# Kernel tuning notes

Hardware: AMD Instinct MI355X
Metric: run time of the kernel (lower is better)

## Reference

```python
import jax, jax.numpy as jnp
import numpy as np

N = 100000
IN_DIM = 256
HID = 128
E = 1600000


def _gcn_conv(x, W, b, src, dst, n_nodes):
    """PyG GCNConv: add self-loops, symmetric normalization, linear transform."""
    xw = x @ W  # [N, H]
    loop = jnp.arange(n_nodes, dtype=src.dtype)
    s = jnp.concatenate([src, loop])  # sources (j)
    d = jnp.concatenate([dst, loop])  # targets (i)
    ones = jnp.ones(s.shape[0], dtype=x.dtype)
    deg = jax.ops.segment_sum(ones, d, num_segments=n_nodes)  # in-degree incl. self-loop
    dinv = jnp.where(deg > 0, jax.lax.rsqrt(deg), 0.0)
    norm = dinv[s] * dinv[d]  # [E+N]
    msgs = xw[s] * norm[:, None]  # gather + scale
    out = jax.ops.segment_sum(msgs, d, num_segments=n_nodes)  # scatter-add at targets
    return out + b


def setup_inputs() -> dict:
    key = jax.random.key(0)
    ks = jax.random.split(key, 12)
    x = jax.random.normal(ks[0], (N, IN_DIM), dtype=jnp.float32)
    edge_index = jax.random.randint(ks[1], (2, E), 0, N, dtype=jnp.int64)
    h_node = jax.random.uniform(ks[2], (N,), dtype=jnp.float32)
    # learned params (glorot-ish scale)
    W1 = jax.random.normal(ks[3], (IN_DIM, HID), dtype=jnp.float32) / np.sqrt(IN_DIM)
    b1 = jnp.zeros((HID,), dtype=jnp.float32)
    W2 = jax.random.normal(ks[4], (HID, HID), dtype=jnp.float32) / np.sqrt(HID)
    b2 = jnp.zeros((HID,), dtype=jnp.float32)
    Wc = jax.random.normal(ks[5], (HID, 2), dtype=jnp.float32) / np.sqrt(HID)
    bc = jnp.zeros((2,), dtype=jnp.float32)
    Wf = jax.random.normal(ks[6], (HID, 2), dtype=jnp.float32) / np.sqrt(HID)
    bf = jnp.zeros((2,), dtype=jnp.float32)
    return {"x": x, "edge_index": edge_index, "h_node": h_node,
            "W1": W1, "b1": b1, "W2": W2, "b2": b2,
            "Wc": Wc, "bc": bc, "Wf": Wf, "bf": bf}


def reference(x, edge_index, h_node, W1, b1, W2, b2, Wc, bc, Wf, bf):
    src, dst = edge_index[0], edge_index[1]
    h1 = jax.nn.relu(_gcn_conv(x, W1, b1, src, dst, x.shape[0]))      # [N, HID]
    logits_coarse = h1 @ Wc + bc                                      # [N, 2]
    alpha = h_node[:, None]                                           # [N, 1]
    h2 = jax.nn.relu(_gcn_conv(h1, W2, b2, src, dst, x.shape[0]))     # [N, HID]
    h2_adaptive = alpha * h2 + (1.0 - alpha) * h1
    logits_fine = h2_adaptive @ Wf + bf                               # [N, 2]
    return 0.5 * logits_coarse + 0.5 * logits_fine
```

## Files before the change

### kernel.cpp

```cpp
#include <hip/hip_runtime.h>


#define HID 128
#define SHIFT 9
#define RANGE 512
#define MAXB 256
#define TILE 4096

typedef __bf16 bf16x8 __attribute__((ext_vector_type(8)));
typedef float  f32x4  __attribute__((ext_vector_type(4)));
typedef float  f32x2  __attribute__((ext_vector_type(2)));

__device__ __forceinline__ unsigned short f2bf(float x) {
    unsigned int b = __float_as_uint(x);
    b += 0x7fffu + ((b >> 16) & 1u);
    return (unsigned short)(b >> 16);
}
__device__ __forceinline__ float bflo(unsigned int u) { return __uint_as_float(u << 16); }
__device__ __forceinline__ float bfhi(unsigned int u) { return __uint_as_float(u & 0xffff0000u); }
__device__ __forceinline__ unsigned packbf(float a, float b) {
    return (unsigned)f2bf(a) | ((unsigned)f2bf(b) << 16);
}


__global__ __launch_bounds__(256)
void bincount_kernel(const int* __restrict__ dst, int* __restrict__ bin_counts,
                     int E, int NB) {
    __shared__ int h[MAXB];
    for (int i = threadIdx.x; i < NB; i += 256) h[i] = 0;
    __syncthreads();
    const int base = blockIdx.x * TILE;
#pragma unroll
    for (int j = 0; j < TILE; j += 256) {
        int e = base + j + threadIdx.x;
        if (e < E) atomicAdd(&h[((unsigned)dst[e]) >> SHIFT], 1);
    }
    __syncthreads();
    for (int i = threadIdx.x; i < NB; i += 256) {
        int v = h[i];
        if (v) atomicAdd(&bin_counts[i], v);
    }
}

__global__ void binscan_kernel(const int* __restrict__ bin_counts,
                               int* __restrict__ bin_off, int* __restrict__ bin_cur, int NB) {
    __shared__ int sh[MAXB];
    const int t = threadIdx.x;
    int v = (t < NB) ? bin_counts[t] : 0;
    sh[t] = v;
    __syncthreads();
    for (int s = 1; s < 256; s <<= 1) {
        int x = (t >= s) ? sh[t - s] : 0;
        __syncthreads();
        sh[t] += x;
        __syncthreads();
    }
    if (t < NB) {
        int ex = sh[t] - v;
        bin_off[t] = ex;
        bin_cur[t] = ex;
    }
}

__global__ __launch_bounds__(256)
void stage_kernel(const int* __restrict__ src, const int* __restrict__ dst,
                  int* __restrict__ bin_cur, unsigned* __restrict__ pairs, int E) {
    __shared__ int sh_hist[MAXB];
    __shared__ int sh_off[MAXB];
    __shared__ int sh_ex[MAXB];
    __shared__ int sh_gbase[MAXB];
    __shared__ uint2 stg[TILE];
    const int t = threadIdx.x;
    const int base = blockIdx.x * TILE;
    const int cnt = min(TILE, E - base);

    for (int i = t; i < MAXB; i += 256) sh_hist[i] = 0;
    __syncthreads();

    int s[16], d[16], r[16];
#pragma unroll
    for (int j = 0; j < 16; ++j) {
        const int k = j * 256 + t;
        if (k < cnt) {
            s[j] = src[base + k];
            d[j] = dst[base + k];
            r[j] = atomicAdd(&sh_hist[((unsigned)d[j]) >> SHIFT], 1);
        }
    }
    __syncthreads();

    const int hv = sh_hist[t];
    sh_off[t] = hv;
    __syncthreads();
    for (int st = 1; st < 256; st <<= 1) {
        int x = (t >= st) ? sh_off[t - st] : 0;
        __syncthreads();
        sh_off[t] += x;
        __syncthreads();
    }
    sh_ex[t] = sh_off[t] - hv;
    if (hv > 0) sh_gbase[t] = atomicAdd(&bin_cur[t], hv);
    __syncthreads();

#pragma unroll
    for (int j = 0; j < 16; ++j) {
        const int k = j * 256 + t;
        if (k < cnt) {
            int b = ((unsigned)d[j]) >> SHIFT;
            stg[sh_ex[b] + r[j]] = make_uint2((unsigned)s[j], (unsigned)d[j]);
        }
    }
    __syncthreads();

    for (int i = t; i < cnt; i += 256) {
        uint2 p = stg[i];
        int b = (int)(p.y >> SHIFT);
        unsigned w = ((p.y & (RANGE - 1)) << 23) | p.x;
        pairs[sh_gbase[b] + (i - sh_ex[b])] = w;
    }
}

__global__ __launch_bounds__(256)
void binrowp_kernel(const unsigned* __restrict__ pairs, const int* __restrict__ bin_off,
                    float* __restrict__ dinv, int* __restrict__ rowp,
                    int N, int NB, int E) {
    __shared__ int c[RANGE];
    __shared__ int sh[256];
    const int b = blockIdx.x;
    const int t = threadIdx.x;
    const int nb = b << SHIFT;
    const int nr = min(RANGE, N - nb);
    for (int i = t; i < RANGE; i += 256) c[i] = 0;
    __syncthreads();
    const int lo = bin_off[b];
    const int hi = (b + 1 < NB) ? bin_off[b + 1] : E;
    for (int i = lo + t; i < hi; i += 256)
        atomicAdd(&c[pairs[i] >> 23], 1);
    __syncthreads();
    const int v0 = c[2 * t], v1 = c[2 * t + 1];
    const int pr = v0 + v1;
    sh[t] = pr;
    __syncthreads();
    for (int s = 1; s < 256; s <<= 1) {
        int x = (t >= s) ? sh[t - s] : 0;
        __syncthreads();
        sh[t] += x;
        __syncthreads();
    }
    const int ex = sh[t] - pr + lo;
    if (2 * t < nr) {
        rowp[nb + 2 * t] = ex;
        dinv[nb + 2 * t] = rsqrtf((float)(v0 + 1));
    }
    if (2 * t + 1 < nr) {
        rowp[nb + 2 * t + 1] = ex + v0;
        dinv[nb + 2 * t + 1] = rsqrtf((float)(v1 + 1));
    }
    if (b == 0 && t == 0) rowp[N] = E;
}

__global__ __launch_bounds__(256)
void fine_kernel(const unsigned* __restrict__ pairs, const int* __restrict__ bin_off,
                 const int* __restrict__ rowp, const float* __restrict__ dinv,
                 unsigned* __restrict__ colv1, int N, int NB, int E) {
    __shared__ int cur[RANGE];
    const int b = blockIdx.x;
    const int nb = b << SHIFT;
    const int nr = min(RANGE, N - nb);
    for (int i = threadIdx.x; i < nr; i += 256) cur[i] = rowp[nb + i];
    __syncthreads();
    const int lo = bin_off[b];
    const int hi = (b + 1 < NB) ? bin_off[b + 1] : E;
    for (int i = lo + threadIdx.x; i < hi; i += 256) {
        unsigned w = pairs[i];
        unsigned s = w & 0x7fffffu;
        int pos = atomicAdd(&cur[w >> 23], 1);
        unsigned w15 = __float2uint_rn(dinv[s] * 32767.0f);
        colv1[pos] = (s << 15) | w15;
    }
}

__global__ void prep_kernel(const float* __restrict__ W1, const float* __restrict__ W2,
                            unsigned short* __restrict__ wt1, unsigned short* __restrict__ wt2,
                            int K1, int* __restrict__ bin_counts) {
    int idx = blockIdx.x * 256 + threadIdx.x;
    if (idx < MAXB) bin_counts[idx] = 0;
    if (idx < 128 * K1) {
        int nn = idx / K1, k = idx - nn * K1;
        wt1[(size_t)nn * K1 + k] = f2bf(W1[(size_t)k * 128 + nn]);
    }
    if (idx < 128 * 128) {
        int nn = idx >> 7, k = idx & 127;
        wt2[(size_t)nn * 128 + k] = f2bf(W2[(size_t)k * 128 + nn]);
    }
}

template <bool A_BF16, int K>
__global__ __launch_bounds__(256)
void gemm_kernel(const void* __restrict__ Aptr, const unsigned short* __restrict__ Wt,
                 unsigned short* __restrict__ Out, int nrows) {
    constexpr int NIT  = K / 32;
    constexpr int DEPTH = (NIT < 4) ? NIT : 4;
    constexpr int HK   = (K > 128) ? (K / 2) : K;
    constexpr int CHH  = HK / 8;
    constexpr int PH   = K / HK;
    constexpr int NITP = HK / 32;
    __shared__ uint4 sB[128 * CHH];

    const int tid  = threadIdx.x;
    const int wave = tid >> 6;
    const int lane = tid & 63;
    const int q = lane >> 4;
    const int r = lane & 15;

    const int wrow = blockIdx.x * 64 + wave * 16;
    const size_t row0 = (size_t)min(wrow + r, nrows - 1);

    const unsigned short* A16 = (const unsigned short*)Aptr;
    const float*          A32 = (const float*)Aptr;

    f32x4 acc[8];
#pragma unroll
    for (int c = 0; c < 8; ++c) acc[c] = (f32x4){0.f, 0.f, 0.f, 0.f};

    bf16x8 preb[DEPTH];
    float4 pref[DEPTH][2];

#pragma unroll
    for (int i = 0; i < DEPTH; ++i) {
        const int kk = i * 32 + q * 8;
        if (A_BF16) {
            preb[i] = *reinterpret_cast<const bf16x8*>(A16 + row0 * K + kk);
        } else {
            pref[i][0] = *reinterpret_cast<const float4*>(A32 + row0 * K + kk);
            pref[i][1] = *reinterpret_cast<const float4*>(A32 + row0 * K + kk + 4);
        }
    }

#pragma unroll
    for (int ph = 0; ph < PH; ++ph) {
        if (ph) __syncthreads();
        for (int idx = tid; idx < 128 * CHH; idx += 256) {
            const int col = idx / CHH;
            const int kc  = idx & (CHH - 1);
            const uint4 v = *reinterpret_cast<const uint4*>(
                Wt + (size_t)col * K + ph * HK + kc * 8);
            sB[col * CHH + (kc ^ (col & (CHH - 1)))] = v;
        }
        __syncthreads();

#pragma unroll
        for (int itp = 0; itp < NITP; ++itp) {
            const int git  = ph * NITP + itp;
            const int slot = git % DEPTH;

            bf16x8 bcur[8];
#pragma unroll
            for (int c = 0; c < 8; ++c) {
                const int col = c * 16 + r;
                const int chunk = (itp * 4 + q) ^ (col & (CHH - 1));
                bcur[c] = *reinterpret_cast<const bf16x8*>(&sB[col * CHH + chunk]);
            }

            bf16x8 afrag;
            if (A_BF16) {
                afrag = preb[slot];
            } else {
                const float4 x0 = pref[slot][0];
                const float4 x1 = pref[slot][1];
                bf16x8 a;
                a[0] = (__bf16)x0.x; a[1] = (__bf16)x0.y; a[2] = (__bf16)x0.z; a[3] = (__bf16)x0.w;
                a[4] = (__bf16)x1.x; a[5] = (__bf16)x1.y; a[6] = (__bf16)x1.z; a[7] = (__bf16)x1.w;
                afrag = a;
            }

            if (git + DEPTH < NIT) {
                const int kk2 = (git + DEPTH) * 32 + q * 8;
                if (A_BF16) {
                    preb[slot] = *reinterpret_cast<const bf16x8*>(A16 + row0 * K + kk2);
                } else {
                    pref[slot][0] = *reinterpret_cast<const float4*>(A32 + row0 * K + kk2);
                    pref[slot][1] = *reinterpret_cast<const float4*>(A32 + row0 * K + kk2 + 4);
                }
            }

#pragma unroll
            for (int c = 0; c < 8; ++c)
                acc[c] = __builtin_amdgcn_mfma_f32_16x16x32_bf16(afrag, bcur[c], acc[c], 0, 0, 0);
        }
    }

#pragma unroll
    for (int v = 0; v < 4; ++v) {
        const int row = wrow + q * 4 + v;
        if (row < nrows) {
#pragma unroll
            for (int c = 0; c < 8; ++c)
                Out[(size_t)row * 128 + c * 16 + r] = f2bf(acc[c][v]);
        }
    }
}


#define AGG_ISSUE(g, TBL)                                                     \
    if ((g) * 4 < cnt) {                                                      \
        _Pragma("unroll")                                                     \
        for (int j = 0; j < 4; ++j) {                                         \
            const int sl = (g) * 4 + j;                                       \
            const unsigned cg = (unsigned)__shfl((int)cw, qb + sl);           \
            wt[sl] = (float)(cg & 0x7fffu) * (1.0f / 32767.0f);               \
            pf[sl] = *reinterpret_cast<const uint4*>(                         \
                (const char*)(TBL) + (((cg >> 15) << 8) + coff));             \
        }                                                                     \
    }

#define AGG_CONS(g)                                                          \
    if ((g) * 4 < cnt) {                                                     \
        _Pragma("unroll")                                                    \
        for (int j = 0; j < 4; ++j) {                                        \
            const int sl = (g) * 4 + j;                                      \
            const float w = wt[sl];                                          \
            const uint4 uu = pf[sl];                                         \
            A0 += (f32x2){bflo(uu.x), bfhi(uu.x)} * w;                       \
            A1 += (f32x2){bflo(uu.y), bfhi(uu.y)} * w;                       \
            A2 += (f32x2){bflo(uu.z), bfhi(uu.z)} * w;                       \
            A3 += (f32x2){bflo(uu.w), bfhi(uu.w)} * w;                       \
        }                                                                    \
    }

#define AGG_EDGE_LOOP(TBL)                                                   \
    unsigned cw = (beg + c < end) ? colv1[beg + c] : 0u;                     \
    for (int base = beg; base < end; base += 16) {                           \
        const int cnt = end - base;                                          \
        AGG_ISSUE(0, TBL) AGG_ISSUE(1, TBL) AGG_ISSUE(2, TBL) AGG_ISSUE(3, TBL) \
        unsigned cw_next = 0u;                                               \
        if (base + 16 + c < end) cw_next = colv1[base + 16 + c];             \
        AGG_CONS(0) AGG_CONS(1) AGG_CONS(2) AGG_CONS(3)                      \
        cw = cw_next;                                                        \
    }

__device__ __forceinline__ f32x2 __shfl_xor(f32x2 v, int m) {
    return (f32x2){__shfl_xor(v[0], m), __shfl_xor(v[1], m)};
}

__global__ __launch_bounds__(256)
void agg1_kernel(const unsigned short* __restrict__ xw, const unsigned* __restrict__ colv1,
                 const int* __restrict__ rowp, const float* __restrict__ dinv,
                 const float* __restrict__ b1, const float* __restrict__ Wc,
                 const float* __restrict__ bc, uint4* __restrict__ h1,
                 float* __restrict__ outp, int n) {
    const int node = blockIdx.x * 16 + (threadIdx.x >> 4);
    if (node >= n) return;
    const int lane = threadIdx.x & 63;
    const int c    = lane & 15;
    const int qb   = lane & 48;
    const unsigned coff = (unsigned)c << 4;
    const float di = dinv[node];
    const int beg = rowp[node], end = rowp[node + 1];

    const uint4 su = *reinterpret_cast<const uint4*>(
        (const char*)xw + (((unsigned)node << 8) + coff));

    f32x2 A0 = {0.f,0.f}, A1 = {0.f,0.f}, A2 = {0.f,0.f}, A3 = {0.f,0.f};
    uint4 pf[16];
    float wt[16];

    AGG_EDGE_LOOP(xw)

    A0 += (f32x2){bflo(su.x), bfhi(su.x)} * di;
    A1 += (f32x2){bflo(su.y), bfhi(su.y)} * di;
    A2 += (f32x2){bflo(su.z), bfhi(su.z)} * di;
    A3 += (f32x2){bflo(su.w), bfhi(su.w)} * di;

    const float4 bb0 = reinterpret_cast<const float4*>(b1)[2*c];
    const float4 bb1 = reinterpret_cast<const float4*>(b1)[2*c + 1];
    float a0 = fmaxf(A0[0]*di + bb0.x, 0.f), a1 = fmaxf(A0[1]*di + bb0.y, 0.f);
    float a2 = fmaxf(A1[0]*di + bb0.z, 0.f), a3 = fmaxf(A1[1]*di + bb0.w, 0.f);
    float a4 = fmaxf(A2[0]*di + bb1.x, 0.f), a5 = fmaxf(A2[1]*di + bb1.y, 0.f);
    float a6 = fmaxf(A3[0]*di + bb1.z, 0.f), a7 = fmaxf(A3[1]*di + bb1.w, 0.f);

    h1[((unsigned)node << 4) + c] =
        make_uint4(packbf(a0,a1), packbf(a2,a3), packbf(a4,a5), packbf(a6,a7));

    const float4 w0 = reinterpret_cast<const float4*>(Wc)[4*c];
    const float4 w1 = reinterpret_cast<const float4*>(Wc)[4*c + 1];
    const float4 w2 = reinterpret_cast<const float4*>(Wc)[4*c + 2];
    const float4 w3 = reinterpret_cast<const float4*>(Wc)[4*c + 3];
    float c0 = a0*w0.x + a1*w0.z + a2*w1.x + a3*w1.z
             + a4*w2.x + a5*w2.z + a6*w3.x + a7*w3.z;
    float c1 = a0*w0.y + a1*w0.w + a2*w1.y + a3*w1.w
             + a4*w2.y + a5*w2.w + a6*w3.y + a7*w3.w;
#pragma unroll
    for (int off = 1; off < 16; off <<= 1) {
        c0 += __shfl_xor(c0, off);
        c1 += __shfl_xor(c1, off);
    }
    if (c == 0) {
        outp[2 * (size_t)node]     = 0.5f * (c0 + bc[0]);
        outp[2 * (size_t)node + 1] = 0.5f * (c1 + bc[1]);
    }
}

__global__ __launch_bounds__(256)
void agg2_kernel(const unsigned short* __restrict__ xw2, const uint4* __restrict__ h1,
                 const unsigned* __restrict__ colv1, const int* __restrict__ rowp,
                 const float* __restrict__ dinv, const float* __restrict__ b2,
                 const float* __restrict__ Wf, const float* __restrict__ bfv,
                 const float* __restrict__ hnode, float* __restrict__ outp, int n) {
    const int node = blockIdx.x * 16 + (threadIdx.x >> 4);
    if (node >= n) return;
    const int lane = threadIdx.x & 63;
    const int c    = lane & 15;
    const int qb   = lane & 48;
    const unsigned coff = (unsigned)c << 4;
    const float di = dinv[node];
    const int beg = rowp[node], end = rowp[node + 1];

    const uint4 su = *reinterpret_cast<const uint4*>(
        (const char*)xw2 + (((unsigned)node << 8) + coff));

    f32x2 A0 = {0.f,0.f}, A1 = {0.f,0.f}, A2 = {0.f,0.f}, A3 = {0.f,0.f};
    uint4 pf[16];
    float wt[16];

    AGG_EDGE_LOOP(xw2)

    A0 += (f32x2){bflo(su.x), bfhi(su.x)} * di;
    A1 += (f32x2){bflo(su.y), bfhi(su.y)} * di;
    A2 += (f32x2){bflo(su.z), bfhi(su.z)} * di;
    A3 += (f32x2){bflo(su.w), bfhi(su.w)} * di;

    const float4 bb0 = reinterpret_cast<const float4*>(b2)[2*c];
    const float4 bb1 = reinterpret_cast<const float4*>(b2)[2*c + 1];
    float h20 = fmaxf(A0[0]*di + bb0.x, 0.f), h21 = fmaxf(A0[1]*di + bb0.y, 0.f);
    float h22 = fmaxf(A1[0]*di + bb0.z, 0.f), h23 = fmaxf(A1[1]*di + bb0.w, 0.f);
    float h24 = fmaxf(A2[0]*di + bb1.x, 0.f), h25 = fmaxf(A2[1]*di + bb1.y, 0.f);
    float h26 = fmaxf(A3[0]*di + bb1.z, 0.f), h27 = fmaxf(A3[1]*di + bb1.w, 0.f);

    const float alpha = hnode[node];
    const float beta  = 1.f - alpha;
    const uint4 hh = h1[((unsigned)node << 4) + c];
    const float ha0 = alpha*h20 + beta*bflo(hh.x);
    const float ha1 = alpha*h21 + beta*bfhi(hh.x);
    const float ha2 = alpha*h22 + beta*bflo(hh.y);
    const float ha3 = alpha*h23 + beta*bfhi(hh.y);
    const float ha4 = alpha*h24 + beta*bflo(hh.z);
    const float ha5 = alpha*h25 + beta*bfhi(hh.z);
    const float ha6 = alpha*h26 + beta*bflo(hh.w);
    const float ha7 = alpha*h27 + beta*bfhi(hh.w);

    const float4 w0 = reinterpret_cast<const float4*>(Wf)[4*c];
    const float4 w1 = reinterpret_cast<const float4*>(Wf)[4*c + 1];
    const float4 w2 = reinterpret_cast<const float4*>(Wf)[4*c + 2];
    const float4 w3 = reinterpret_cast<const float4*>(Wf)[4*c + 3];
    float f0 = ha0*w0.x + ha1*w0.z + ha2*w1.x + ha3*w1.z
             + ha4*w2.x + ha5*w2.z + ha6*w3.x + ha7*w3.z;
    float f1 = ha0*w0.y + ha1*w0.w + ha2*w1.y + ha3*w1.w
             + ha4*w2.y + ha5*w2.w + ha6*w3.y + ha7*w3.w;
#pragma unroll
    for (int off = 1; off < 16; off <<= 1) {
        f0 += __shfl_xor(f0, off);
        f1 += __shfl_xor(f1, off);
    }
    if (c == 0) {
        outp[2 * (size_t)node]     += 0.5f * (f0 + bfv[0]);
        outp[2 * (size_t)node + 1] += 0.5f * (f1 + bfv[1]);
    }
}


extern "C" void kernel_launch(void* const* d_in, const int* in_sizes, int n_in,
                              void* d_out, int out_size, void* d_ws, size_t ws_size,
                              hipStream_t stream) {
    const float* x     = (const float*)d_in[0];
    const int*   ei    = (const int*)d_in[1];
    const float* hnode = (const float*)d_in[2];
    const float* W1    = (const float*)d_in[3];
    const float* b1    = (const float*)d_in[4];
    const float* W2    = (const float*)d_in[5];
    const float* b2    = (const float*)d_in[6];
    const float* Wc    = (const float*)d_in[7];
    const float* bc    = (const float*)d_in[8];
    const float* Wf    = (const float*)d_in[9];
    const float* bfv   = (const float*)d_in[10];

    const int N  = in_sizes[2];
    const int E  = in_sizes[1] / 2;
    const int K1 = in_sizes[3] / HID;
    const int NB = (N + RANGE - 1) >> SHIFT;
    const int* srcv = ei;
    const int* dstv = ei + E;
    float* outp = (float*)d_out;

    char* ws = (char*)d_ws;
    size_t off = 0;
    auto alloc = [&](size_t bytes) -> char* {
        char* p = ws + off;
        off += (bytes + 255) & ~(size_t)255;
        return p;
    };
    unsigned short* xw       = (unsigned short*)alloc((size_t)N * HID * 2);
    unsigned short* h1       = (unsigned short*)alloc((size_t)N * HID * 2);
    float*          dinv     = (float*)alloc((size_t)N * 4);
    int*            rowp     = (int*)alloc((size_t)(N + 1) * 4);
    unsigned*       colv1    = (unsigned*)alloc((size_t)E * 4);
    unsigned*       pairs    = (unsigned*)alloc((size_t)E * 4);
    int*            bin_counts = (int*)alloc(MAXB * 4);
    int*            bin_off    = (int*)alloc(MAXB * 4);
    int*            bin_cur    = (int*)alloc(MAXB * 4);
    unsigned short* wt1      = (unsigned short*)alloc((size_t)HID * K1 * 2);
    unsigned short* wt2      = (unsigned short*)alloc((size_t)HID * HID * 2);

    prep_kernel<<<(HID * K1 + 255) / 256, 256, 0, stream>>>(W1, W2, wt1, wt2, K1, bin_counts);

    const int ntiles = (E + TILE - 1) / TILE;
    bincount_kernel<<<ntiles, 256, 0, stream>>>(dstv, bin_counts, E, NB);
    binscan_kernel<<<1, 256, 0, stream>>>(bin_counts, bin_off, bin_cur, NB);
    stage_kernel<<<ntiles, 256, 0, stream>>>(srcv, dstv, bin_cur, pairs, E);
    binrowp_kernel<<<NB, 256, 0, stream>>>(pairs, bin_off, dinv, rowp, N, NB, E);
    fine_kernel<<<NB, 256, 0, stream>>>(pairs, bin_off, rowp, dinv, colv1, N, NB, E);

    gemm_kernel<false, 256><<<(N + 63) / 64, 256, 0, stream>>>((const void*)x, wt1, xw, N);
    agg1_kernel<<<(N + 15) / 16, 256, 0, stream>>>(xw, colv1, rowp, dinv,
                                                   b1, Wc, bc, (uint4*)h1, outp, N);
    gemm_kernel<true, 128><<<(N + 63) / 64, 256, 0, stream>>>((const void*)h1, wt2, xw, N);
    agg2_kernel<<<(N + 15) / 16, 256, 0, stream>>>(xw, (const uint4*)h1, colv1,
                                                   rowp, dinv, b2, Wf, bfv, hnode, outp, N);
}
```

Before: 375.8 us.

## Use 8 lanes per node with double-buffered edge gathers in aggregation

Both aggregation kernels now map each node to 8 lanes instead of 16, so each lane gathers 32 bytes (two uint4) per neighbor row and 32 nodes fit in a block. The edge loop becomes a two-stage software pipeline with ping-pong prefetch buffers and sched_barriers, and it recomputes weights from the shuffled column word instead of storing them. The aim is to halve the lanes per node, which doubles node-level parallelism per wave, and to overlap gather latency with accumulation. The trade-off is higher register pressure from 16 prefetched uint4 plus 16 accumulators, which may reduce occupancy.

Result: slower. 393.1 us (+4.6%).

```diff
diff --git a/kernel.cpp b/kernel.cpp
--- a/kernel.cpp
+++ b/kernel.cpp
@@ -302,41 +302,61 @@
 }
 
 
-#define AGG_ISSUE(g, TBL)                                                     \
-    if ((g) * 4 < cnt) {                                                      \
+#define AGG_ISS(PF, CW, t)                                                    \
+    if (((t) << 2) < me) {                                                    \
         _Pragma("unroll")                                                     \
         for (int j = 0; j < 4; ++j) {                                         \
-            const int sl = (g) * 4 + j;                                       \
-            const unsigned cg = (unsigned)__shfl((int)cw, qb + sl);           \
-            wt[sl] = (float)(cg & 0x7fffu) * (1.0f / 32767.0f);               \
-            pf[sl] = *reinterpret_cast<const uint4*>(                         \
-                (const char*)(TBL) + (((cg >> 15) << 8) + coff));             \
+            const unsigned cg = (unsigned)__shfl((int)(CW), gb + j);          \
+            const char* p = (const char*)tbl + (((cg >> 15) << 8) + coff);    \
+            PF[2 * j]     = *reinterpret_cast<const uint4*>(p);               \
+            PF[2 * j + 1] = *reinterpret_cast<const uint4*>(p + 16);          \
         }                                                                     \
     }
 
-#define AGG_CONS(g)                                                          \
-    if ((g) * 4 < cnt) {                                                     \
-        _Pragma("unroll")                                                    \
-        for (int j = 0; j < 4; ++j) {                                        \
-            const int sl = (g) * 4 + j;                                      \
-            const float w = wt[sl];                                          \
-            const uint4 uu = pf[sl];                                         \
-            A0 += (f32x2){bflo(uu.x), bfhi(uu.x)} * w;                       \
-            A1 += (f32x2){bflo(uu.y), bfhi(uu.y)} * w;                       \
-            A2 += (f32x2){bflo(uu.z), bfhi(uu.z)} * w;                       \
-            A3 += (f32x2){bflo(uu.w), bfhi(uu.w)} * w;                       \
-        }                                                                    \
-    }
-
-#define AGG_EDGE_LOOP(TBL)                                                   \
-    unsigned cw = (beg + c < end) ? colv1[beg + c] : 0u;                     \
-    for (int base = beg; base < end; base += 16) {                           \
-        const int cnt = end - base;                                          \
-        AGG_ISSUE(0, TBL) AGG_ISSUE(1, TBL) AGG_ISSUE(2, TBL) AGG_ISSUE(3, TBL) \
-        unsigned cw_next = 0u;                                               \
-        if (base + 16 + c < end) cw_next = colv1[base + 16 + c];             \
-        AGG_CONS(0) AGG_CONS(1) AGG_CONS(2) AGG_CONS(3)                      \
-        cw = cw_next;                                                        \
+#define AGG_CNS(PF, CW, t)                                                    \
+    if (((t) << 2) < me) {                                                    \
+        _Pragma("unroll")                                                     \
+        for (int j = 0; j < 4; ++j) {                                         \
+            const unsigned cg = (unsigned)__shfl((int)(CW), gb + j);          \
+            const float w = (float)(cg & 0x7fffu) * (1.0f / 32767.0f);        \
+            const uint4 u0 = PF[2 * j];                                       \
+            const uint4 u1 = PF[2 * j + 1];                                   \
+            A0 += (f32x2){bflo(u0.x), bfhi(u0.x)} * w;                        \
+            A1 += (f32x2){bflo(u0.y), bfhi(u0.y)} * w;                        \
+            A2 += (f32x2){bflo(u0.z), bfhi(u0.z)} * w;                        \
+            A3 += (f32x2){bflo(u0.w), bfhi(u0.w)} * w;                        \
+            A4 += (f32x2){bflo(u1.x), bfhi(u1.x)} * w;                        \
+            A5 += (f32x2){bflo(u1.y), bfhi(u1.y)} * w;                        \
+            A6 += (f32x2){bflo(u1.z), bfhi(u1.z)} * w;                        \
+            A7 += (f32x2){bflo(u1.w), bfhi(u1.w)} * w;                        \
+        }                                                                     \
+    }
+
+#define AGG_EDGE_LOOP(TBL)                                                    \
+    const unsigned short* tbl = (TBL);                                        \
+    const int me = end - beg;                                                 \
+    auto ldcv = [&](int t) -> unsigned {                                      \
+        const int idx = beg + (t << 2) + (c8 & 3);                            \
+        return (idx < end) ? colv1[idx] : 0u;                                 \
+    };                                                                        \
+    uint4 pfA[8], pfB[8];                                                     \
+    unsigned cw0 = ldcv(0);                                                   \
+    unsigned cw1 = ldcv(1);                                                   \
+    AGG_ISS(pfA, cw0, 0)                                                      \
+    const int mych = (me + 3) >> 2;                                           \
+    for (int t = 0; t < mych; t += 2) {                                       \
+        const unsigned cw2 = ldcv(t + 2);                                     \
+        __builtin_amdgcn_sched_barrier(0);                                    \
+        AGG_ISS(pfB, cw1, t + 1)                                              \
+        __builtin_amdgcn_sched_barrier(0);                                    \
+        AGG_CNS(pfA, cw0, t)                                                  \
+        const unsigned cw3 = ldcv(t + 3);                                     \
+        __builtin_amdgcn_sched_barrier(0);                                    \
+        AGG_ISS(pfA, cw2, t + 2)                                              \
+        __builtin_amdgcn_sched_barrier(0);                                    \
+        AGG_CNS(pfB, cw1, t + 1)                                              \
+        __builtin_amdgcn_sched_barrier(0);                                    \
+        cw0 = cw2; cw1 = cw3;                                                 \
     }
 
 __device__ __forceinline__ f32x2 __shfl_xor(f32x2 v, int m) {
@@ -349,53 +369,66 @@
                  const float* __restrict__ b1, const float* __restrict__ Wc,
                  const float* __restrict__ bc, uint4* __restrict__ h1,
                  float* __restrict__ outp, int n) {
-    const int node = blockIdx.x * 16 + (threadIdx.x >> 4);
+    const int node = blockIdx.x * 32 + (threadIdx.x >> 3);
     if (node >= n) return;
     const int lane = threadIdx.x & 63;
-    const int c    = lane & 15;
-    const int qb   = lane & 48;
-    const unsigned coff = (unsigned)c << 4;
+    const int c8   = lane & 7;
+    const int gb   = lane & 56;
+    const unsigned coff = (unsigned)c8 << 5;
     const float di = dinv[node];
     const int beg = rowp[node], end = rowp[node + 1];
 
-    const uint4 su = *reinterpret_cast<const uint4*>(
-        (const char*)xw + (((unsigned)node << 8) + coff));
+    const char* sp = (const char*)xw + (((unsigned)node << 8) + coff);
+    const uint4 su0 = *reinterpret_cast<const uint4*>(sp);
+    const uint4 su1 = *reinterpret_cast<const uint4*>(sp + 16);
 
     f32x2 A0 = {0.f,0.f}, A1 = {0.f,0.f}, A2 = {0.f,0.f}, A3 = {0.f,0.f};
-    uint4 pf[16];
-    float wt[16];
+    f32x2 A4 = {0.f,0.f}, A5 = {0.f,0.f}, A6 = {0.f,0.f}, A7 = {0.f,0.f};
 
     AGG_EDGE_LOOP(xw)
 
-    A0 += (f32x2){bflo(su.x), bfhi(su.x)} * di;
-    A1 += (f32x2){bflo(su.y), bfhi(su.y)} * di;
-    A2 += (f32x2){bflo(su.z), bfhi(su.z)} * di;
-    A3 += (f32x2){bflo(su.w), bfhi(su.w)} * di;
-
-    const float4 bb0 = reinterpret_cast<const float4*>(b1)[2*c];
-    const float4 bb1 = reinterpret_cast<const float4*>(b1)[2*c + 1];
-    float a0 = fmaxf(A0[0]*di + bb0.x, 0.f), a1 = fmaxf(A0[1]*di + bb0.y, 0.f);
-    float a2 = fmaxf(A1[0]*di + bb0.z, 0.f), a3 = fmaxf(A1[1]*di + bb0.w, 0.f);
-    float a4 = fmaxf(A2[0]*di + bb1.x, 0.f), a5 = fmaxf(A2[1]*di + bb1.y, 0.f);
-    float a6 = fmaxf(A3[0]*di + bb1.z, 0.f), a7 = fmaxf(A3[1]*di + bb1.w, 0.f);
-
-    h1[((unsigned)node << 4) + c] =
+    A0 += (f32x2){bflo(su0.x), bfhi(su0.x)} * di;
+    A1 += (f32x2){bflo(su0.y), bfhi(su0.y)} * di;
+    A2 += (f32x2){bflo(su0.z), bfhi(su0.z)} * di;
+    A3 += (f32x2){bflo(su0.w), bfhi(su0.w)} * di;
+    A4 += (f32x2){bflo(su1.x), bfhi(su1.x)} * di;
+    A5 += (f32x2){bflo(su1.y), bfhi(su1.y)} * di;
+    A6 += (f32x2){bflo(su1.z), bfhi(su1.z)} * di;
+    A7 += (f32x2){bflo(su1.w), bfhi(su1.w)} * di;
+
+    const float4* b4 = reinterpret_cast<const float4*>(b1);
+    const float4 bb0 = b4[4*c8], bb1 = b4[4*c8+1], bb2 = b4[4*c8+2], bb3 = b4[4*c8+3];
+    float a0  = fmaxf(A0[0]*di + bb0.x, 0.f), a1  = fmaxf(A0[1]*di + bb0.y, 0.f);
+    float a2  = fmaxf(A1[0]*di + bb0.z, 0.f), a3  = fmaxf(A1[1]*di + bb0.w, 0.f);
+    float a4  = fmaxf(A2[0]*di + bb1.x, 0.f), a5  = fmaxf(A2[1]*di + bb1.y, 0.f);
+    float a6  = fmaxf(A3[0]*di + bb1.z, 0.f), a7  = fmaxf(A3[1]*di + bb1.w, 0.f);
+    float a8  = fmaxf(A4[0]*di + bb2.x, 0.f), a9  = fmaxf(A4[1]*di + bb2.y, 0.f);
+    float a10 = fmaxf(A5[0]*di + bb2.z, 0.f), a11 = fmaxf(A5[1]*di + bb2.w, 0.f);
+    float a12 = fmaxf(A6[0]*di + bb3.x, 0.f), a13 = fmaxf(A6[1]*di + bb3.y, 0.f);
+    float a14 = fmaxf(A7[0]*di + bb3.z, 0.f), a15 = fmaxf(A7[1]*di + bb3.w, 0.f);
+
+    h1[((unsigned)node << 4) + 2*c8] =
         make_uint4(packbf(a0,a1), packbf(a2,a3), packbf(a4,a5), packbf(a6,a7));
-
-    const float4 w0 = reinterpret_cast<const float4*>(Wc)[4*c];
-    const float4 w1 = reinterpret_cast<const float4*>(Wc)[4*c + 1];
-    const float4 w2 = reinterpret_cast<const float4*>(Wc)[4*c + 2];
-    const float4 w3 = reinterpret_cast<const float4*>(Wc)[4*c + 3];
-    float c0 = a0*w0.x + a1*w0.z + a2*w1.x + a3*w1.z
-             + a4*w2.x + a5*w2.z + a6*w3.x + a7*w3.z;
-    float c1 = a0*w0.y + a1*w0.w + a2*w1.y + a3*w1.w
-             + a4*w2.y + a5*w2.w + a6*w3.y + a7*w3.w;
-#pragma unroll
-    for (int off = 1; off < 16; off <<= 1) {
+    h1[((unsigned)node << 4) + 2*c8 + 1] =
+        make_uint4(packbf(a8,a9), packbf(a10,a11), packbf(a12,a13), packbf(a14,a15));
+
+    const float4* w4 = reinterpret_cast<const float4*>(Wc);
+    float c0 = 0.f, c1 = 0.f;
+    {
+        const float av[16] = {a0,a1,a2,a3,a4,a5,a6,a7,a8,a9,a10,a11,a12,a13,a14,a15};
+#pragma unroll
+        for (int j = 0; j < 8; ++j) {
+            const float4 w = w4[8*c8 + j];
+            c0 += av[2*j]*w.x + av[2*j+1]*w.z;
+            c1 += av[2*j]*w.y + av[2*j+1]*w.w;
+        }
+    }
+#pragma unroll
+    for (int off = 1; off < 8; off <<= 1) {
         c0 += __shfl_xor(c0, off);
         c1 += __shfl_xor(c1, off);
     }
-    if (c == 0) {
+    if (c8 == 0) {
         outp[2 * (size_t)node]     = 0.5f * (c0 + bc[0]);
         outp[2 * (size_t)node + 1] = 0.5f * (c1 + bc[1]);
     }
@@ -407,62 +440,73 @@
                  const float* __restrict__ dinv, const float* __restrict__ b2,
                  const float* __restrict__ Wf, const float* __restrict__ bfv,
                  const float* __restrict__ hnode, float* __restrict__ outp, int n) {
-    const int node = blockIdx.x * 16 + (threadIdx.x >> 4);
+    const int node = blockIdx.x * 32 + (threadIdx.x >> 3);
     if (node >= n) return;
     const int lane = threadIdx.x & 63;
-    const int c    = lane & 15;
-    const int qb   = lane & 48;
-    const unsigned coff = (unsigned)c << 4;
+    const int c8   = lane & 7;
+    const int gb   = lane & 56;
+    const unsigned coff = (unsigned)c8 << 5;
     const float di = dinv[node];
     const int beg = rowp[node], end = rowp[node + 1];
 
-    const uint4 su = *reinterpret_cast<const uint4*>(
-        (const char*)xw2 + (((unsigned)node << 8) + coff));
+    const char* sp = (const char*)xw2 + (((unsigned)node << 8) + coff);
+    const uint4 su0 = *reinterpret_cast<const uint4*>(sp);
+    const uint4 su1 = *reinterpret_cast<const uint4*>(sp + 16);
 
     f32x2 A0 = {0.f,0.f}, A1 = {0.f,0.f}, A2 = {0.f,0.f}, A3 = {0.f,0.f};
-    uint4 pf[16];
-    float wt[16];
+    f32x2 A4 = {0.f,0.f}, A5 = {0.f,0.f}, A6 = {0.f,0.f}, A7 = {0.f,0.f};
 
     AGG_EDGE_LOOP(xw2)
 
-    A0 += (f32x2){bflo(su.x), bfhi(su.x)} * di;
-    A1 += (f32x2){bflo(su.y), bfhi(su.y)} * di;
-    A2 += (f32x2){bflo(su.z), bfhi(su.z)} * di;
-    A3 += (f32x2){bflo(su.w), bfhi(su.w)} * di;
-
-    const float4 bb0 = reinterpret_cast<const float4*>(b2)[2*c];
-    const float4 bb1 = reinterpret_cast<const float4*>(b2)[2*c + 1];
-    float h20 = fmaxf(A0[0]*di + bb0.x, 0.f), h21 = fmaxf(A0[1]*di + bb0.y, 0.f);
-    float h22 = fmaxf(A1[0]*di + bb0.z, 0.f), h23 = fmaxf(A1[1]*di + bb0.w, 0.f);
-    float h24 = fmaxf(A2[0]*di + bb1.x, 0.f), h25 = fmaxf(A2[1]*di + bb1.y, 0.f);
-    float h26 = fmaxf(A3[0]*di + bb1.z, 0.f), h27 = fmaxf(A3[1]*di + bb1.w, 0.f);
+    A0 += (f32x2){bflo(su0.x), bfhi(su0.x)} * di;
+    A1 += (f32x2){bflo(su0.y), bfhi(su0.y)} * di;
+    A2 += (f32x2){bflo(su0.z), bfhi(su0.z)} * di;
+    A3 += (f32x2){bflo(su0.w), bfhi(su0.w)} * di;
+    A4 += (f32x2){bflo(su1.x), bfhi(su1.x)} * di;
+    A5 += (f32x2){bflo(su1.y), bfhi(su1.y)} * di;
+    A6 += (f32x2){bflo(su1.z), bfhi(su1.z)} * di;
+    A7 += (f32x2){bflo(su1.w), bfhi(su1.w)} * di;
+
+    const float4* b4 = reinterpret_cast<const float4*>(b2);
+    const float4 bb0 = b4[4*c8], bb1 = b4[4*c8+1], bb2 = b4[4*c8+2], bb3 = b4[4*c8+3];
+    float h2v[16];
+    h2v[0]  = fmaxf(A0[0]*di + bb0.x, 0.f); h2v[1]  = fmaxf(A0[1]*di + bb0.y, 0.f);
+    h2v[2]  = fmaxf(A1[0]*di + bb0.z, 0.f); h2v[3]  = fmaxf(A1[1]*di + bb0.w, 0.f);
+    h2v[4]  = fmaxf(A2[0]*di + bb1.x, 0.f); h2v[5]  = fmaxf(A2[1]*di + bb1.y, 0.f);
+    h2v[6]  = fmaxf(A3[0]*di + bb1.z, 0.f); h2v[7]  = fmaxf(A3[1]*di + bb1.w, 0.f);
+    h2v[8]  = fmaxf(A4[0]*di + bb2.x, 0.f); h2v[9]  = fmaxf(A4[1]*di + bb2.y, 0.f);
+    h2v[10] = fmaxf(A5[0]*di + bb2.z, 0.f); h2v[11] = fmaxf(A5[1]*di + bb2.w, 0.f);
+    h2v[12] = fmaxf(A6[0]*di + bb3.x, 0.f); h2v[13] = fmaxf(A6[1]*di + bb3.y, 0.f);
+    h2v[14] = fmaxf(A7[0]*di + bb3.z, 0.f); h2v[15] = fmaxf(A7[1]*di + bb3.w, 0.f);
 
     const float alpha = hnode[node];
     const float beta  = 1.f - alpha;
-    const uint4 hh = h1[((unsigned)node << 4) + c];
-    const float ha0 = alpha*h20 + beta*bflo(hh.x);
-    const float ha1 = alpha*h21 + beta*bfhi(hh.x);
-    const float ha2 = alpha*h22 + beta*bflo(hh.y);
-    const float ha3 = alpha*h23 + beta*bfhi(hh.y);
-    const float ha4 = alpha*h24 + beta*bflo(hh.z);
-    const float ha5 = alpha*h25 + beta*bfhi(hh.z);
-    const float ha6 = alpha*h26 + beta*bflo(hh.w);
-    const float ha7 = alpha*h27 + beta*bfhi(hh.w);
-
-    const float4 w0 = reinterpret_cast<const float4*>(Wf)[4*c];
-    const float4 w1 = reinterpret_cast<const float4*>(Wf)[4*c + 1];
-    const float4 w2 = reinterpret_cast<const float4*>(Wf)[4*c + 2];
-    const float4 w3 = reinterpret_cast<const float4*>(Wf)[4*c + 3];
-    float f0 = ha0*w0.x + ha1*w0.z + ha2*w1.x + ha3*w1.z
-             + ha4*w2.x + ha5*w2.z + ha6*w3.x + ha7*w3.z;
-    float f1 = ha0*w0.y + ha1*w0.w + ha2*w1.y + ha3*w1.w
-             + ha4*w2.y + ha5*w2.w + ha6*w3.y + ha7*w3.w;
-#pragma unroll
-    for (int off = 1; off < 16; off <<= 1) {
+    const uint4 hh0 = h1[((unsigned)node << 4) + 2*c8];
+    const uint4 hh1 = h1[((unsigned)node << 4) + 2*c8 + 1];
+    float ha[16];
+    ha[0]  = alpha*h2v[0]  + beta*bflo(hh0.x); ha[1]  = alpha*h2v[1]  + beta*bfhi(hh0.x);
+    ha[2]  = alpha*h2v[2]  + beta*bflo(hh0.y); ha[3]  = alpha*h2v[3]  + beta*bfhi(hh0.y);
+    ha[4]  = alpha*h2v[4]  + beta*bflo(hh0.z); ha[5]  = alpha*h2v[5]  + beta*bfhi(hh0.z);
+    ha[6]  = alpha*h2v[6]  + beta*bflo(hh0.w); ha[7]  = alpha*h2v[7]  + beta*bfhi(hh0.w);
+    ha[8]  = alpha*h2v[8]  + beta*bflo(hh1.x); ha[9]  = alpha*h2v[9]  + beta*bfhi(hh1.x);
+    ha[10] = alpha*h2v[10] + beta*bflo(hh1.y); ha[11] = alpha*h2v[11] + beta*bfhi(hh1.y);
+    ha[12] = alpha*h2v[12] + beta*bflo(hh1.z); ha[13] = alpha*h2v[13] + beta*bfhi(hh1.z);
+    ha[14] = alpha*h2v[14] + beta*bflo(hh1.w); ha[15] = alpha*h2v[15] + beta*bfhi(hh1.w);
+
+    const float4* w4 = reinterpret_cast<const float4*>(Wf);
+    float f0 = 0.f, f1 = 0.f;
+#pragma unroll
+    for (int j = 0; j < 8; ++j) {
+        const float4 w = w4[8*c8 + j];
+        f0 += ha[2*j]*w.x + ha[2*j+1]*w.z;
+        f1 += ha[2*j]*w.y + ha[2*j+1]*w.w;
+    }
+#pragma unroll
+    for (int off = 1; off < 8; off <<= 1) {
         f0 += __shfl_xor(f0, off);
         f1 += __shfl_xor(f1, off);
     }
-    if (c == 0) {
+    if (c8 == 0) {
         outp[2 * (size_t)node]     += 0.5f * (f0 + bfv[0]);
         outp[2 * (size_t)node + 1] += 0.5f * (f1 + bfv[1]);
     }
@@ -521,9 +565,9 @@
     fine_kernel<<<NB, 256, 0, stream>>>(pairs, bin_off, rowp, dinv, colv1, N, NB, E);
 
     gemm_kernel<false, 256><<<(N + 63) / 64, 256, 0, stream>>>((const void*)x, wt1, xw, N);
-    agg1_kernel<<<(N + 15) / 16, 256, 0, stream>>>(xw, colv1, rowp, dinv,
+    agg1_kernel<<<(N + 31) / 32, 256, 0, stream>>>(xw, colv1, rowp, dinv,
                                                    b1, Wc, bc, (uint4*)h1, outp, N);
     gemm_kernel<true, 128><<<(N + 63) / 64, 256, 0, stream>>>((const void*)h1, wt2, xw, N);
-    agg2_kernel<<<(N + 15) / 16, 256, 0, stream>>>(xw, (const uint4*)h1, colv1,
+    agg2_kernel<<<(N + 31) / 32, 256, 0, stream>>>(xw, (const uint4*)h1, colv1,
                                                    rowp, dinv, b2, Wf, bfv, hnode, outp, N);
 }
```

## Fold source-side dinv scaling into GEMM epilogue and use persistent aggregation loops

Applied to the files above, without the earlier changes.

Moves the per-source normalization factor dinv[s] out of the edge lists and into the GEMM output, so each row of xw is pre-scaled. The edge entries become plain column indices, which removes the quantized weight decode and the multiply from the aggregation inner loop, and removes the dinv gather from fine_kernel. Padding lanes now point at a zeroed dummy row N instead of row 0. The aggregation kernels become grid-stride loops with a capped grid, and the self-loop term now reads the already-scaled row. This trades some launch and tail behavior for fewer per-edge ALU operations, and it also drops the 15-bit weight quantization error.

Result: no change. 381.1 us (+1.4%).

```diff
diff --git a/kernel.cpp b/kernel.cpp
--- a/kernel.cpp
+++ b/kernel.cpp
@@ -173,18 +173,18 @@
     const int hi = (b + 1 < NB) ? bin_off[b + 1] : E;
     for (int i = lo + threadIdx.x; i < hi; i += 256) {
         unsigned w = pairs[i];
-        unsigned s = w & 0x7fffffu;
         int pos = atomicAdd(&cur[w >> 23], 1);
-        unsigned w15 = __float2uint_rn(dinv[s] * 32767.0f);
-        colv1[pos] = (s << 15) | w15;
+        colv1[pos] = w & 0x7fffffu;
     }
 }
 
 __global__ void prep_kernel(const float* __restrict__ W1, const float* __restrict__ W2,
                             unsigned short* __restrict__ wt1, unsigned short* __restrict__ wt2,
-                            int K1, int* __restrict__ bin_counts) {
+                            int K1, int* __restrict__ bin_counts,
+                            unsigned short* __restrict__ xw_pad, int N) {
     int idx = blockIdx.x * 256 + threadIdx.x;
     if (idx < MAXB) bin_counts[idx] = 0;
+    if (idx < HID) xw_pad[(size_t)N * HID + idx] = 0;
     if (idx < 128 * K1) {
         int nn = idx / K1, k = idx - nn * K1;
         wt1[(size_t)nn * K1 + k] = f2bf(W1[(size_t)k * 128 + nn]);
@@ -198,7 +198,8 @@
 template <bool A_BF16, int K>
 __global__ __launch_bounds__(256)
 void gemm_kernel(const void* __restrict__ Aptr, const unsigned short* __restrict__ Wt,
-                 unsigned short* __restrict__ Out, int nrows) {
+                 const float* __restrict__ dinvv, unsigned short* __restrict__ Out,
+                 int nrows) {
     constexpr int NIT  = K / 32;
     constexpr int DEPTH = (NIT < 4) ? NIT : 4;
     constexpr int HK   = (K > 128) ? (K / 2) : K;
@@ -294,9 +295,10 @@
     for (int v = 0; v < 4; ++v) {
         const int row = wrow + q * 4 + v;
         if (row < nrows) {
+            const float sc = dinvv[row];
 #pragma unroll
             for (int c = 0; c < 8; ++c)
-                Out[(size_t)row * 128 + c * 16 + r] = f2bf(acc[c][v]);
+                Out[(size_t)row * 128 + c * 16 + r] = f2bf(acc[c][v] * sc);
         }
     }
 }
@@ -308,9 +310,8 @@
         for (int j = 0; j < 4; ++j) {                                         \
             const int sl = (g) * 4 + j;                                       \
             const unsigned cg = (unsigned)__shfl((int)cw, qb + sl);           \
-            wt[sl] = (float)(cg & 0x7fffu) * (1.0f / 32767.0f);               \
             pf[sl] = *reinterpret_cast<const uint4*>(                         \
-                (const char*)(TBL) + (((cg >> 15) << 8) + coff));             \
+                (const char*)(TBL) + (((size_t)cg << 8) + coff));             \
         }                                                                     \
     }
 
@@ -318,23 +319,21 @@
     if ((g) * 4 < cnt) {                                                     \
         _Pragma("unroll")                                                    \
         for (int j = 0; j < 4; ++j) {                                        \
-            const int sl = (g) * 4 + j;                                      \
-            const float w = wt[sl];                                          \
-            const uint4 uu = pf[sl];                                         \
-            A0 += (f32x2){bflo(uu.x), bfhi(uu.x)} * w;                       \
-            A1 += (f32x2){bflo(uu.y), bfhi(uu.y)} * w;                       \
-            A2 += (f32x2){bflo(uu.z), bfhi(uu.z)} * w;                       \
-            A3 += (f32x2){bflo(uu.w), bfhi(uu.w)} * w;                       \
+            const uint4 uu = pf[(g) * 4 + j];                                \
+            A0 += (f32x2){bflo(uu.x), bfhi(uu.x)};                           \
+            A1 += (f32x2){bflo(uu.y), bfhi(uu.y)};                           \
+            A2 += (f32x2){bflo(uu.z), bfhi(uu.z)};                           \
+            A3 += (f32x2){bflo(uu.w), bfhi(uu.w)};                           \
         }                                                                    \
     }
 
 #define AGG_EDGE_LOOP(TBL)                                                   \
-    unsigned cw = (beg + c < end) ? colv1[beg + c] : 0u;                     \
-    for (int base = beg; base < end; base += 16) {                           \
-        const int cnt = end - base;                                          \
+    unsigned cw = (beg + c < end) ? colv1[beg + c] : (unsigned)n;            \
+    for (int eb = beg; eb < end; eb += 16) {                                 \
+        const int cnt = end - eb;                                            \
         AGG_ISSUE(0, TBL) AGG_ISSUE(1, TBL) AGG_ISSUE(2, TBL) AGG_ISSUE(3, TBL) \
-        unsigned cw_next = 0u;                                               \
-        if (base + 16 + c < end) cw_next = colv1[base + 16 + c];             \
+        unsigned cw_next = (unsigned)n;                                      \
+        if (eb + 16 + c < end) cw_next = colv1[eb + 16 + c];                 \
         AGG_CONS(0) AGG_CONS(1) AGG_CONS(2) AGG_CONS(3)                      \
         cw = cw_next;                                                        \
     }
@@ -349,55 +348,63 @@
                  const float* __restrict__ b1, const float* __restrict__ Wc,
                  const float* __restrict__ bc, uint4* __restrict__ h1,
                  float* __restrict__ outp, int n) {
-    const int node = blockIdx.x * 16 + (threadIdx.x >> 4);
-    if (node >= n) return;
     const int lane = threadIdx.x & 63;
+    const int wid  = threadIdx.x >> 6;
     const int c    = lane & 15;
+    const int q4   = lane >> 4;
     const int qb   = lane & 48;
     const unsigned coff = (unsigned)c << 4;
-    const float di = dinv[node];
-    const int beg = rowp[node], end = rowp[node + 1];
-
-    const uint4 su = *reinterpret_cast<const uint4*>(
-        (const char*)xw + (((unsigned)node << 8) + coff));
-
-    f32x2 A0 = {0.f,0.f}, A1 = {0.f,0.f}, A2 = {0.f,0.f}, A3 = {0.f,0.f};
-    uint4 pf[16];
-    float wt[16];
-
-    AGG_EDGE_LOOP(xw)
-
-    A0 += (f32x2){bflo(su.x), bfhi(su.x)} * di;
-    A1 += (f32x2){bflo(su.y), bfhi(su.y)} * di;
-    A2 += (f32x2){bflo(su.z), bfhi(su.z)} * di;
-    A3 += (f32x2){bflo(su.w), bfhi(su.w)} * di;
-
-    const float4 bb0 = reinterpret_cast<const float4*>(b1)[2*c];
-    const float4 bb1 = reinterpret_cast<const float4*>(b1)[2*c + 1];
-    float a0 = fmaxf(A0[0]*di + bb0.x, 0.f), a1 = fmaxf(A0[1]*di + bb0.y, 0.f);
-    float a2 = fmaxf(A1[0]*di + bb0.z, 0.f), a3 = fmaxf(A1[1]*di + bb0.w, 0.f);
-    float a4 = fmaxf(A2[0]*di + bb1.x, 0.f), a5 = fmaxf(A2[1]*di + bb1.y, 0.f);
-    float a6 = fmaxf(A3[0]*di + bb1.z, 0.f), a7 = fmaxf(A3[1]*di + bb1.w, 0.f);
-
-    h1[((unsigned)node << 4) + c] =
-        make_uint4(packbf(a0,a1), packbf(a2,a3), packbf(a4,a5), packbf(a6,a7));
-
-    const float4 w0 = reinterpret_cast<const float4*>(Wc)[4*c];
-    const float4 w1 = reinterpret_cast<const float4*>(Wc)[4*c + 1];
-    const float4 w2 = reinterpret_cast<const float4*>(Wc)[4*c + 2];
-    const float4 w3 = reinterpret_cast<const float4*>(Wc)[4*c + 3];
-    float c0 = a0*w0.x + a1*w0.z + a2*w1.x + a3*w1.z
-             + a4*w2.x + a5*w2.z + a6*w3.x + a7*w3.z;
-    float c1 = a0*w0.y + a1*w0.w + a2*w1.y + a3*w1.w
-             + a4*w2.y + a5*w2.w + a6*w3.y + a7*w3.w;
-#pragma unroll
-    for (int off = 1; off < 16; off <<= 1) {
-        c0 += __shfl_xor(c0, off);
-        c1 += __shfl_xor(c1, off);
-    }
-    if (c == 0) {
-        outp[2 * (size_t)node]     = 0.5f * (c0 + bc[0]);
-        outp[2 * (size_t)node + 1] = 0.5f * (c1 + bc[1]);
+
+    for (int bn = blockIdx.x * 16 + wid * 4; bn < n; bn += gridDim.x * 16) {
+        const int node = bn + q4;
+        const bool act = node < n;
+        const int nc   = act ? node : (n - 1);
+        const float di = act ? dinv[nc] : 0.f;
+        const int beg = act ? rowp[nc] : 0;
+        const int end = act ? rowp[nc + 1] : 0;
+
+        const float ws = act ? 1.f : 0.f;
+        const uint4 su = *reinterpret_cast<const uint4*>(
+            (const char*)xw + (((size_t)nc << 8) + coff));
+
+        f32x2 A0 = {0.f,0.f}, A1 = {0.f,0.f}, A2 = {0.f,0.f}, A3 = {0.f,0.f};
+        uint4 pf[16];
+
+        AGG_EDGE_LOOP(xw)
+
+        A0 += (f32x2){bflo(su.x), bfhi(su.x)} * ws;
+        A1 += (f32x2){bflo(su.y), bfhi(su.y)} * ws;
+        A2 += (f32x2){bflo(su.z), bfhi(su.z)} * ws;
+        A3 += (f32x2){bflo(su.w), bfhi(su.w)} * ws;
+
+        const float4 bb0 = reinterpret_cast<const float4*>(b1)[2*c];
+        const float4 bb1 = reinterpret_cast<const float4*>(b1)[2*c + 1];
+        float a0 = fmaxf(A0[0]*di + bb0.x, 0.f), a1 = fmaxf(A0[1]*di + bb0.y, 0.f);
+        float a2 = fmaxf(A1[0]*di + bb0.z, 0.f), a3 = fmaxf(A1[1]*di + bb0.w, 0.f);
+        float a4 = fmaxf(A2[0]*di + bb1.x, 0.f), a5 = fmaxf(A2[1]*di + bb1.y, 0.f);
+        float a6 = fmaxf(A3[0]*di + bb1.z, 0.f), a7 = fmaxf(A3[1]*di + bb1.w, 0.f);
+
+        if (act)
+            h1[((size_t)nc << 4) + c] =
+                make_uint4(packbf(a0,a1), packbf(a2,a3), packbf(a4,a5), packbf(a6,a7));
+
+        const float4 w0 = reinterpret_cast<const float4*>(Wc)[4*c];
+        const float4 w1 = reinterpret_cast<const float4*>(Wc)[4*c + 1];
+        const float4 w2 = reinterpret_cast<const float4*>(Wc)[4*c + 2];
+        const float4 w3 = reinterpret_cast<const float4*>(Wc)[4*c + 3];
+        float c0 = a0*w0.x + a1*w0.z + a2*w1.x + a3*w1.z
+                 + a4*w2.x + a5*w2.z + a6*w3.x + a7*w3.z;
+        float c1 = a0*w0.y + a1*w0.w + a2*w1.y + a3*w1.w
+                 + a4*w2.y + a5*w2.w + a6*w3.y + a7*w3.w;
+#pragma unroll
+        for (int off = 1; off < 16; off <<= 1) {
+            c0 += __shfl_xor(c0, off);
+            c1 += __shfl_xor(c1, off);
+        }
+        if (act && c == 0) {
+            outp[2 * (size_t)nc]     = 0.5f * (c0 + bc[0]);
+            outp[2 * (size_t)nc + 1] = 0.5f * (c1 + bc[1]);
+        }
     }
 }
 
@@ -407,64 +414,71 @@
                  const float* __restrict__ dinv, const float* __restrict__ b2,
                  const float* __restrict__ Wf, const float* __restrict__ bfv,
                  const float* __restrict__ hnode, float* __restrict__ outp, int n) {
-    const int node = blockIdx.x * 16 + (threadIdx.x >> 4);
-    if (node >= n) return;
     const int lane = threadIdx.x & 63;
+    const int wid  = threadIdx.x >> 6;
     const int c    = lane & 15;
+    const int q4   = lane >> 4;
     const int qb   = lane & 48;
     const unsigned coff = (unsigned)c << 4;
-    const float di = dinv[node];
-    const int beg = rowp[node], end = rowp[node + 1];
-
-    const uint4 su = *reinterpret_cast<const uint4*>(
-        (const char*)xw2 + (((unsigned)node << 8) + coff));
-
-    f32x2 A0 = {0.f,0.f}, A1 = {0.f,0.f}, A2 = {0.f,0.f}, A3 = {0.f,0.f};
-    uint4 pf[16];
-    float wt[16];
-
-    AGG_EDGE_LOOP(xw2)
-
-    A0 += (f32x2){bflo(su.x), bfhi(su.x)} * di;
-    A1 += (f32x2){bflo(su.y), bfhi(su.y)} * di;
-    A2 += (f32x2){bflo(su.z), bfhi(su.z)} * di;
-    A3 += (f32x2){bflo(su.w), bfhi(su.w)} * di;
-
-    const float4 bb0 = reinterpret_cast<const float4*>(b2)[2*c];
-    const float4 bb1 = reinterpret_cast<const float4*>(b2)[2*c + 1];
-    float h20 = fmaxf(A0[0]*di + bb0.x, 0.f), h21 = fmaxf(A0[1]*di + bb0.y, 0.f);
-    float h22 = fmaxf(A1[0]*di + bb0.z, 0.f), h23 = fmaxf(A1[1]*di + bb0.w, 0.f);
-    float h24 = fmaxf(A2[0]*di + bb1.x, 0.f), h25 = fmaxf(A2[1]*di + bb1.y, 0.f);
-    float h26 = fmaxf(A3[0]*di + bb1.z, 0.f), h27 = fmaxf(A3[1]*di + bb1.w, 0.f);
-
-    const float alpha = hnode[node];
-    const float beta  = 1.f - alpha;
-    const uint4 hh = h1[((unsigned)node << 4) + c];
-    const float ha0 = alpha*h20 + beta*bflo(hh.x);
-    const float ha1 = alpha*h21 + beta*bfhi(hh.x);
-    const float ha2 = alpha*h22 + beta*bflo(hh.y);
-    const float ha3 = alpha*h23 + beta*bfhi(hh.y);
-    const float ha4 = alpha*h24 + beta*bflo(hh.z);
-    const float ha5 = alpha*h25 + beta*bfhi(hh.z);
-    const float ha6 = alpha*h26 + beta*bflo(hh.w);
-    const float ha7 = alpha*h27 + beta*bfhi(hh.w);
-
-    const float4 w0 = reinterpret_cast<const float4*>(Wf)[4*c];
-    const float4 w1 = reinterpret_cast<const float4*>(Wf)[4*c + 1];
-    const float4 w2 = reinterpret_cast<const float4*>(Wf)[4*c + 2];
-    const float4 w3 = reinterpret_cast<const float4*>(Wf)[4*c + 3];
-    float f0 = ha0*w0.x + ha1*w0.z + ha2*w1.x + ha3*w1.z
-             + ha4*w2.x + ha5*w2.z + ha6*w3.x + ha7*w3.z;
-    float f1 = ha0*w0.y + ha1*w0.w + ha2*w1.y + ha3*w1.w
-             + ha4*w2.y + ha5*w2.w + ha6*w3.y + ha7*w3.w;
-#pragma unroll
-    for (int off = 1; off < 16; off <<= 1) {
-        f0 += __shfl_xor(f0, off);
-        f1 += __shfl_xor(f1, off);
-    }
-    if (c == 0) {
-        outp[2 * (size_t)node]     += 0.5f * (f0 + bfv[0]);
-        outp[2 * (size_t)node + 1] += 0.5f * (f1 + bfv[1]);
+
+    for (int bn = blockIdx.x * 16 + wid * 4; bn < n; bn += gridDim.x * 16) {
+        const int node = bn + q4;
+        const bool act = node < n;
+        const int nc   = act ? node : (n - 1);
+        const float di = act ? dinv[nc] : 0.f;
+        const int beg = act ? rowp[nc] : 0;
+        const int end = act ? rowp[nc + 1] : 0;
+
+        const float ws = act ? 1.f : 0.f;
+        const uint4 su = *reinterpret_cast<const uint4*>(
+            (const char*)xw2 + (((size_t)nc << 8) + coff));
+
+        f32x2 A0 = {0.f,0.f}, A1 = {0.f,0.f}, A2 = {0.f,0.f}, A3 = {0.f,0.f};
+        uint4 pf[16];
+
+        AGG_EDGE_LOOP(xw2)
+
+        A0 += (f32x2){bflo(su.x), bfhi(su.x)} * ws;
+        A1 += (f32x2){bflo(su.y), bfhi(su.y)} * ws;
+        A2 += (f32x2){bflo(su.z), bfhi(su.z)} * ws;
+        A3 += (f32x2){bflo(su.w), bfhi(su.w)} * ws;
+
+        const float4 bb0 = reinterpret_cast<const float4*>(b2)[2*c];
+        const float4 bb1 = reinterpret_cast<const float4*>(b2)[2*c + 1];
+        float h20 = fmaxf(A0[0]*di + bb0.x, 0.f), h21 = fmaxf(A0[1]*di + bb0.y, 0.f);
+        float h22 = fmaxf(A1[0]*di + bb0.z, 0.f), h23 = fmaxf(A1[1]*di + bb0.w, 0.f);
+        float h24 = fmaxf(A2[0]*di + bb1.x, 0.f), h25 = fmaxf(A2[1]*di + bb1.y, 0.f);
+        float h26 = fmaxf(A3[0]*di + bb1.z, 0.f), h27 = fmaxf(A3[1]*di + bb1.w, 0.f);
+
+        const float alpha = act ? hnode[nc] : 0.f;
+        const float beta  = 1.f - alpha;
+        const uint4 hh = h1[((size_t)nc << 4) + c];
+        const float ha0 = alpha*h20 + beta*bflo(hh.x);
+        const float ha1 = alpha*h21 + beta*bfhi(hh.x);
+        const float ha2 = alpha*h22 + beta*bflo(hh.y);
+        const float ha3 = alpha*h23 + beta*bfhi(hh.y);
+        const float ha4 = alpha*h24 + beta*bflo(hh.z);
+        const float ha5 = alpha*h25 + beta*bfhi(hh.z);
+        const float ha6 = alpha*h26 + beta*bflo(hh.w);
+        const float ha7 = alpha*h27 + beta*bfhi(hh.w);
+
+        const float4 w0 = reinterpret_cast<const float4*>(Wf)[4*c];
+        const float4 w1 = reinterpret_cast<const float4*>(Wf)[4*c + 1];
+        const float4 w2 = reinterpret_cast<const float4*>(Wf)[4*c + 2];
+        const float4 w3 = reinterpret_cast<const float4*>(Wf)[4*c + 3];
+        float f0 = ha0*w0.x + ha1*w0.z + ha2*w1.x + ha3*w1.z
+                 + ha4*w2.x + ha5*w2.z + ha6*w3.x + ha7*w3.z;
+        float f1 = ha0*w0.y + ha1*w0.w + ha2*w1.y + ha3*w1.w
+                 + ha4*w2.y + ha5*w2.w + ha6*w3.y + ha7*w3.w;
+#pragma unroll
+        for (int off = 1; off < 16; off <<= 1) {
+            f0 += __shfl_xor(f0, off);
+            f1 += __shfl_xor(f1, off);
+        }
+        if (act && c == 0) {
+            outp[2 * (size_t)nc]     += 0.5f * (f0 + bfv[0]);
+            outp[2 * (size_t)nc + 1] += 0.5f * (f1 + bfv[1]);
+        }
     }
 }
 
@@ -499,7 +513,7 @@
         off += (bytes + 255) & ~(size_t)255;
         return p;
     };
-    unsigned short* xw       = (unsigned short*)alloc((size_t)N * HID * 2);
+    unsigned short* xw       = (unsigned short*)alloc((size_t)(N + 1) * HID * 2);
     unsigned short* h1       = (unsigned short*)alloc((size_t)N * HID * 2);
     float*          dinv     = (float*)alloc((size_t)N * 4);
     int*            rowp     = (int*)alloc((size_t)(N + 1) * 4);
@@ -511,7 +525,8 @@
     unsigned short* wt1      = (unsigned short*)alloc((size_t)HID * K1 * 2);
     unsigned short* wt2      = (unsigned short*)alloc((size_t)HID * HID * 2);
 
-    prep_kernel<<<(HID * K1 + 255) / 256, 256, 0, stream>>>(W1, W2, wt1, wt2, K1, bin_counts);
+    prep_kernel<<<(HID * K1 + 255) / 256, 256, 0, stream>>>(W1, W2, wt1, wt2, K1,
+                                                            bin_counts, xw, N);
 
     const int ntiles = (E + TILE - 1) / TILE;
     bincount_kernel<<<ntiles, 256, 0, stream>>>(dstv, bin_counts, E, NB);
@@ -520,10 +535,11 @@
     binrowp_kernel<<<NB, 256, 0, stream>>>(pairs, bin_off, dinv, rowp, N, NB, E);
     fine_kernel<<<NB, 256, 0, stream>>>(pairs, bin_off, rowp, dinv, colv1, N, NB, E);
 
-    gemm_kernel<false, 256><<<(N + 63) / 64, 256, 0, stream>>>((const void*)x, wt1, xw, N);
-    agg1_kernel<<<(N + 15) / 16, 256, 0, stream>>>(xw, colv1, rowp, dinv,
-                                                   b1, Wc, bc, (uint4*)h1, outp, N);
-    gemm_kernel<true, 128><<<(N + 63) / 64, 256, 0, stream>>>((const void*)h1, wt2, xw, N);
-    agg2_kernel<<<(N + 15) / 16, 256, 0, stream>>>(xw, (const uint4*)h1, colv1,
-                                                   rowp, dinv, b2, Wf, bfv, hnode, outp, N);
-}
+    const int agrid = min((N + 15) / 16, 2048);
+    gemm_kernel<false, 256><<<(N + 63) / 64, 256, 0, stream>>>((const void*)x, wt1, dinv, xw, N);
+    agg1_kernel<<<agrid, 256, 0, stream>>>(xw, colv1, rowp, dinv,
+                                           b1, Wc, bc, (uint4*)h1, outp, N);
+    gemm_kernel<true, 128><<<(N + 63) / 64, 256, 0, stream>>>((const void*)h1, wt2, dinv, xw, N);
+    agg2_kernel<<<agrid, 256, 0, stream>>>(xw, (const uint4*)h1, colv1,
+                                           rowp, dinv, b2, Wf, bfv, hnode, outp, N);
+}
```
